# Performance work log

Hardware: AMD Instinct MI355X
Metric: run time of the kernel (lower is better)

Reference implementation:

```python
import jax, jax.numpy as jnp
import numpy as np

# fixed 9 neighborhood offsets (center + 8 directions), in pixel units
BASE = np.array([[0,0],[-1,-1],[0,-1],[1,-1],[-1,0],[1,0],[-1,1],[0,1],[1,1]], dtype=np.float32)
MAX_DELTA = 0.5 / 512.0


def bilinear_sample(vm, gx, gy):
    """vm: (D,H,W); gx,gy: (N,) normalized grid coords in [-1,1].
    Bilinear, padding_mode='zeros', align_corners=True. Returns (D,N)."""
    D, H, W = vm.shape
    ix = (gx + 1.0) * 0.5 * (W - 1)
    iy = (gy + 1.0) * 0.5 * (H - 1)
    x0 = jnp.floor(ix); y0 = jnp.floor(iy)
    x1 = x0 + 1.0;      y1 = y0 + 1.0
    wx1 = ix - x0; wx0 = 1.0 - wx1
    wy1 = iy - y0; wy0 = 1.0 - wy1
    fm = vm.reshape(D, H * W)

    def corner(xf, yf, wx, wy):
        valid = (xf >= 0) & (xf <= W - 1) & (yf >= 0) & (yf <= H - 1)
        xi = jnp.clip(xf.astype(jnp.int32), 0, W - 1)
        yi = jnp.clip(yf.astype(jnp.int32), 0, H - 1)
        v = jnp.take(fm, yi * W + xi, axis=1)  # (D,N) gather
        w = jnp.where(valid, wx * wy, 0.0)
        return v * w

    return (corner(x0, y0, wx0, wy0) + corner(x1, y0, wx1, wy0)
            + corner(x0, y1, wx0, wy1) + corner(x1, y1, wx1, wy1))


def setup_inputs() -> dict:
    key = jax.random.key(0)
    ks = jax.random.split(key, 5)
    B, C, Hf, Wf = 4, 256, 128, 128
    T, D = 16384, 128
    fmap = jax.random.normal(ks[0], (B, C, Hf, Wf), dtype=jnp.float32)
    coords = jax.random.uniform(ks[1], (B, T, 2), dtype=jnp.float32)
    W_proj = jax.random.normal(ks[2], (D, C), dtype=jnp.float32) * (1.0 / np.sqrt(C))
    W1 = jax.random.normal(ks[3], (D, D), dtype=jnp.float32) * (1.0 / np.sqrt(D))
    b1 = jnp.zeros((D,), dtype=jnp.float32)
    W2 = jax.random.normal(ks[4], (2, D), dtype=jnp.float32) * (1.0 / np.sqrt(D))
    b2 = jnp.zeros((2,), dtype=jnp.float32)
    return {"fmap": fmap, "coords": coords, "W_proj": W_proj,
            "W1": W1, "b1": b1, "W2": W2, "b2": b2}


def reference(fmap, coords, W_proj, W1, b1, W2, b2):
    B, C, Hf, Wf = fmap.shape
    T = coords.shape[1]
    K = BASE.shape[0]
    # 1x1 conv projection
    vm = jnp.einsum('bchw,dc->bdhw', fmap, W_proj)  # (B,D,Hf,Wf)
    # offsets: one pixel step in [0,1] coords (align_corners=True)
    step = jnp.array([1.0 / (Wf - 1), 1.0 / (Hf - 1)], dtype=coords.dtype)
    grid = coords[:, :, None, :] + jnp.asarray(BASE)[None, None] * step  # (B,T,K,2)
    grid = grid * 2.0 - 1.0                                            # normalize to [-1,1]
    grid = grid.reshape(B, T * K, 2)
    feat = jax.vmap(bilinear_sample)(vm, grid[..., 0], grid[..., 1])   # (B,D,T*K)
    D = feat.shape[1]
    feat = feat.transpose(0, 2, 1).reshape(B, T, K, D).mean(axis=2)    # (B,T,D)
    h = jax.nn.relu(feat @ W1.T + b1)
    delta = jnp.tanh(h @ W2.T + b2) * MAX_DELTA
    return coords + delta
```

## Files before the change

kernel.cpp:

```cpp
#include <hip/hip_runtime.h>
#include <cstddef>

#define NB 4
#define NC 256
#define ND 128
#define NH 128
#define NW 128
#define NHW (NH*NW)
#define NT 16384
#define NBKT 1024
#define CAP 192
#define FS 136

typedef short   short8  __attribute__((ext_vector_type(8)));
typedef unsigned short ushort8 __attribute__((ext_vector_type(8)));
typedef float   floatx4 __attribute__((ext_vector_type(4)));
typedef float   floatx2 __attribute__((ext_vector_type(2)));

__device__ __forceinline__ unsigned pk_bf16(float a, float b) {
    unsigned ua = __float_as_uint(a);
    unsigned ub = __float_as_uint(b);
    ua += 0x7fffu + ((ua >> 16) & 1u);
    ub += 0x7fffu + ((ub >> 16) & 1u);
    return (ua >> 16) | (ub & 0xffff0000u);
}

__device__ __forceinline__ unsigned fp8x4_from_f32(float v0, float v1, float v2, float v3) {
    int r = 0;
    r = __builtin_amdgcn_cvt_pk_fp8_f32(v0, v1, r, false);
    r = __builtin_amdgcn_cvt_pk_fp8_f32(v2, v3, r, true);
    return (unsigned)r;
}
template <bool HI>
__device__ __forceinline__ floatx2 fp8x2_to_f32(unsigned w) {
    return __builtin_amdgcn_cvt_pk_f32_fp8((int)w, HI);
}

__device__ __forceinline__ int bucket_of(float cx, float cy, int b) {
    int x0 = (int)floorf(cx * (float)(NW - 1));
    int y0 = (int)floorf(cy * (float)(NH - 1));
    x0 = min(max(x0, 0), NW - 1);
    y0 = min(max(y0, 0), NH - 1);
    return b * 256 + (y0 >> 3) * 16 + (x0 >> 3);
}

__global__ __launch_bounds__(1024)
void fill_kernel(const float* __restrict__ coords, const float* __restrict__ W1,
                 int* __restrict__ counts, int* __restrict__ order,
                 unsigned short* __restrict__ W1bf)
{
    const int bi = blockIdx.x;
    if (bi >= 64) {
        const int i = (bi - 64) * 1024 + threadIdx.x;
        unsigned u = __float_as_uint(W1[i]);
        u += 0x7fffu + ((u >> 16) & 1u);
        W1bf[i] = (unsigned short)(u >> 16);
        return;
    }
    const int g = bi * 1024 + threadIdx.x;
    const float cx = coords[(size_t)g*2 + 0];
    const float cy = coords[(size_t)g*2 + 1];
    const int bkt = bucket_of(cx, cy, g >> 14);
    const int pos = atomicAdd(&counts[bkt], 1);
    if (pos < CAP) order[bkt*CAP + pos] = g;
}

__global__ __launch_bounds__(512, 4)
void proj_kernel(const float* __restrict__ fmap, const float* __restrict__ Wp,
                 unsigned char* __restrict__ vm)
{
    const int bi = blockIdx.x;
    __shared__ unsigned short awp[8*8*64*8];

    const int t    = threadIdx.x;
    const int lane = t & 63;
    const int w    = t >> 6;
    const int l15  = lane & 15;
    const int q    = lane >> 4;
    const int cq   = q * 8;

    {
        const int dt = w;
        const float* wr0 = Wp + (size_t)(dt*16 + l15)*NC + cq;
        #pragma unroll
        for (int ch = 0; ch < 8; ++ch) {
            float4 g0 = *(const float4*)(wr0 + ch*32);
            float4 g1 = *(const float4*)(wr0 + ch*32 + 4);
            uint4 pk = make_uint4(pk_bf16(g0.x,g0.y), pk_bf16(g0.z,g0.w),
                                  pk_bf16(g1.x,g1.y), pk_bf16(g1.z,g1.w));
            *(uint4*)&awp[((dt*8 + ch)*64 + lane)*8] = pk;
        }
    }
    __syncthreads();

    const int b    = (bi & 7) >> 1;
    const int slot = ((bi >> 3) << 1) | (bi & 1);
    const int p    = slot*128 + w*16 + l15;

    floatx4 acc[8];
    #pragma unroll
    for (int i = 0; i < 8; ++i) acc[i] = (floatx4)(0.f);

    const float* fbase = fmap + (size_t)b*NC*NHW + p;

    #pragma unroll
    for (int c0 = 0; c0 < 8; ++c0) {
        const float* bp = fbase + (size_t)(c0*32 + cq)*NHW;
        float f[8];
        #pragma unroll
        for (int j = 0; j < 8; ++j) f[j] = bp[(size_t)j*NHW];
        union { short8 v; unsigned u[4]; } bc;
        #pragma unroll
        for (int j = 0; j < 4; ++j) bc.u[j] = pk_bf16(f[2*j], f[2*j+1]);
        #pragma unroll
        for (int dt = 0; dt < 8; ++dt) {
            short8 afr = *(const short8*)&awp[((dt*8 + c0)*64 + lane)*8];
            acc[dt] = __builtin_amdgcn_mfma_f32_16x16x32_bf16(afr, bc.v, acc[dt], 0, 0, 0);
        }
    }
    unsigned char* vrow = vm + ((size_t)(b*NHW + p))*ND;
    #pragma unroll
    for (int dt = 0; dt < 8; ++dt) {
        floatx4 v = acc[dt];
        *(unsigned*)&vrow[dt*16 + q*4] = fp8x4_from_f32(v[0], v[1], v[2], v[3]);
    }
}

__global__ __launch_bounds__(512, 4)
void gather_mlp(const unsigned char* __restrict__ vm, const float* __restrict__ coords,
                const int* __restrict__ counts, const int* __restrict__ order,
                const unsigned short* __restrict__ W1bf, const float* __restrict__ b1,
                const float* __restrict__ W2, const float* __restrict__ b2,
                float* __restrict__ out)
{
    __shared__ unsigned short feat[64 * FS];
    __shared__ float part[64][8];
    __shared__ float W2s[256];
    __shared__ float b1s[128];
    __shared__ int gidx[64];
    const int t   = threadIdx.x;
    const int bkt = blockIdx.x;
    const int n      = min(counts[bkt], CAP);
    const int chunks = (n + 63) >> 6;

    if (t < 128) {
        W2s[t*2]   = W2[t];
        W2s[t*2+1] = W2[ND + t];
        b1s[t]     = b1[t];
    }
    __syncthreads();

    for (int c = 0; c < chunks; ++c) {
        const int np = min(n - c*64, 64);

        {
            const int pt = t >> 3;
            const int c8 = t & 7;
            if (pt < np) {
                const int g = order[bkt*CAP + c*64 + pt];
                if (c8 == 0) gidx[pt] = g;
                const int b = g >> 14;
                const float cx = coords[(size_t)g*2 + 0];
                const float cy = coords[(size_t)g*2 + 1];
                const float ix = cx * (float)(NW - 1);
                const float iy = cy * (float)(NH - 1);
                const float x0f = floorf(ix), y0f = floorf(iy);
                const int x0 = (int)x0f, y0 = (int)y0f;
                const float wx1 = ix - x0f, wy1 = iy - y0f;
                const float wxv[4] = {1.f - wx1, 1.f, 1.f, wx1};
                const float wyv[4] = {1.f - wy1, 1.f, 1.f, wy1};
                floatx2 acc[8];
                #pragma unroll
                for (int k = 0; k < 8; ++k) acc[k] = (floatx2)(0.f);
                const unsigned char* vmb = vm + (size_t)b*NHW*ND + c8*16;
                #pragma unroll
                for (int j = 0; j < 4; ++j) {
                    const int Y  = y0 - 1 + j;
                    const int Yc = min(max(Y, 0), NH-1);
                    const bool vy = (Y >= 0) & (Y < NH);
                    #pragma unroll
                    for (int i = 0; i < 4; ++i) {
                        const int X  = x0 - 1 + i;
                        const int Xc = min(max(X, 0), NW-1);
                        const bool vx = (X >= 0) & (X < NW);
                        const float wgt = (vx & vy) ? wxv[i]*wyv[j] : 0.f;
                        uint4 u = *(const uint4*)(vmb + (size_t)(Yc*NW + Xc)*ND);
                        const floatx2 w2 = {wgt, wgt};
                        acc[0] += w2 * fp8x2_to_f32<false>(u.x);
                        acc[1] += w2 * fp8x2_to_f32<true >(u.x);
                        acc[2] += w2 * fp8x2_to_f32<false>(u.y);
                        acc[3] += w2 * fp8x2_to_f32<true >(u.y);
                        acc[4] += w2 * fp8x2_to_f32<false>(u.z);
                        acc[5] += w2 * fp8x2_to_f32<true >(u.z);
                        acc[6] += w2 * fp8x2_to_f32<false>(u.w);
                        acc[7] += w2 * fp8x2_to_f32<true >(u.w);
                    }
                }
                const float s9 = 1.f/9.f;
                unsigned pk[8];
                #pragma unroll
                for (int k = 0; k < 8; ++k)
                    pk[k] = pk_bf16(acc[k].x*s9, acc[k].y*s9);
                *(uint4*)&feat[pt*FS + c8*16]     = make_uint4(pk[0],pk[1],pk[2],pk[3]);
                *(uint4*)&feat[pt*FS + c8*16 + 8] = make_uint4(pk[4],pk[5],pk[6],pk[7]);
            }
        }
        __syncthreads();

        {
            const int lane = t & 63;
            const int w    = t >> 6;
            const int l15  = lane & 15;
            const int q    = lane >> 4;
            const int mp   = w & 3;
            const int npr  = w >> 2;

            floatx4 C[2][2];
            #pragma unroll
            for (int mi = 0; mi < 2; ++mi)
                #pragma unroll
                for (int ni = 0; ni < 2; ++ni) C[mi][ni] = (floatx4)(0.f);

            #pragma unroll
            for (int kk = 0; kk < 4; ++kk) {
                short8 a0 = *(const short8*)&W1bf[((mp*2+0)*16 + l15)*ND + kk*32 + q*8];
                short8 a1 = *(const short8*)&W1bf[((mp*2+1)*16 + l15)*ND + kk*32 + q*8];
                short8 f0 = *(const short8*)&feat[((npr*2+0)*16 + l15)*FS + kk*32 + q*8];
                short8 f1 = *(const short8*)&feat[((npr*2+1)*16 + l15)*FS + kk*32 + q*8];
                C[0][0] = __builtin_amdgcn_mfma_f32_16x16x32_bf16(a0, f0, C[0][0], 0, 0, 0);
                C[0][1] = __builtin_amdgcn_mfma_f32_16x16x32_bf16(a0, f1, C[0][1], 0, 0, 0);
                C[1][0] = __builtin_amdgcn_mfma_f32_16x16x32_bf16(a1, f0, C[1][0], 0, 0, 0);
                C[1][1] = __builtin_amdgcn_mfma_f32_16x16x32_bf16(a1, f1, C[1][1], 0, 0, 0);
            }
            #pragma unroll
            for (int ni = 0; ni < 2; ++ni) {
                float s0 = 0.f, s1 = 0.f;
                #pragma unroll
                for (int mi = 0; mi < 2; ++mi) {
                    const int e0 = (mp*2 + mi)*16 + q*4;
                    float4 bq = *(const float4*)&b1s[e0];
                    floatx4 h4 = C[mi][ni];
                    #pragma unroll
                    for (int r = 0; r < 4; ++r) {
                        float hv = fmaxf(h4[r] + (&bq.x)[r], 0.f);
                        float2 wv = *(const float2*)&W2s[(e0 + r)*2];
                        s0 = fmaf(hv, wv.x, s0);
                        s1 = fmaf(hv, wv.y, s1);
                    }
                }
                s0 += __shfl_xor(s0, 16); s0 += __shfl_xor(s0, 32);
                s1 += __shfl_xor(s1, 16); s1 += __shfl_xor(s1, 32);
                if (q == 0) {
                    const int pt = (npr*2 + ni)*16 + l15;
                    part[pt][mp*2 + 0] = s0;
                    part[pt][mp*2 + 1] = s1;
                }
            }
        }
        __syncthreads();

        if (t < np) {
            const int g = gidx[t];
            float s0 = part[t][0] + part[t][2] + part[t][4] + part[t][6];
            float s1 = part[t][1] + part[t][3] + part[t][5] + part[t][7];
            const float cx = coords[(size_t)g*2 + 0];
            const float cy = coords[(size_t)g*2 + 1];
            const float MD = 0.5f / 512.0f;
            float2 o = make_float2(cx + tanhf(s0 + b2[0]) * MD,
                                   cy + tanhf(s1 + b2[1]) * MD);
            *(float2*)&out[(size_t)g*2] = o;
        }
        __syncthreads();
    }
}

extern "C" void kernel_launch(void* const* d_in, const int* in_sizes, int n_in,
                              void* d_out, int out_size, void* d_ws, size_t ws_size,
                              hipStream_t stream)
{
    const float* fmap   = (const float*)d_in[0];
    const float* coords = (const float*)d_in[1];
    const float* Wp     = (const float*)d_in[2];
    const float* W1     = (const float*)d_in[3];
    const float* b1     = (const float*)d_in[4];
    const float* W2     = (const float*)d_in[5];
    const float* b2     = (const float*)d_in[6];
    float* out = (float*)d_out;

    unsigned char* vm = (unsigned char*)d_ws;
    char* base = (char*)d_ws + (size_t)NB*NHW*ND;
    unsigned short* W1bf = (unsigned short*)base;
    int* counts = (int*)(base + 32768);
    int* order  = (int*)(base + 32768 + 4096);

    hipMemsetAsync(counts, 0, NBKT*sizeof(int), stream);
    fill_kernel<<<dim3(64 + 16), 1024, 0, stream>>>(coords, W1, counts, order, W1bf);
    proj_kernel<<<dim3(512),      512, 0, stream>>>(fmap, Wp, vm);
    gather_mlp <<<dim3(NBKT),     512, 0, stream>>>(vm, coords, counts, order,
                                                    W1bf, b1, W2, b2, out);
}
```

Measured before the change: 152.6 us.

## Split bucket chunks into a work queue and precompute bf16 projection weights

Each bucket's chunks of up to 64 points now become separate queue entries, built by an extra block in the projection kernel. The gather/MLP kernel launches one block per queue entry instead of looping over chunks inside one block per bucket, which spreads uneven bucket loads across more blocks. The fp32-to-bf16 conversion and swizzle of the projection weights moves into the fill kernel, so each projection block only copies the packed weights into shared memory. In exchange it adds a queue-building pass and atomics, launches up to 3072 blocks that early-exit when unused, and spends extra workspace.

```diff
diff --git a/kernel.cpp b/kernel.cpp
--- a/kernel.cpp
+++ b/kernel.cpp
@@ -11,6 +11,7 @@
 #define NBKT 1024
 #define CAP 192
 #define FS 136
+#define MAXQ 3072
 
 typedef short   short8  __attribute__((ext_vector_type(8)));
 typedef unsigned short ushort8 __attribute__((ext_vector_type(8)));
@@ -46,18 +47,34 @@
 
 __global__ __launch_bounds__(1024)
 void fill_kernel(const float* __restrict__ coords, const float* __restrict__ W1,
+                 const float* __restrict__ Wp,
                  int* __restrict__ counts, int* __restrict__ order,
-                 unsigned short* __restrict__ W1bf)
+                 unsigned short* __restrict__ W1bf, unsigned short* __restrict__ Wpbf)
 {
     const int bi = blockIdx.x;
+    const int t  = threadIdx.x;
+    if (bi >= 80) {
+        const int idx  = (bi - 80) * 1024 + t;
+        const int lane = idx & 63;
+        const int ch   = (idx >> 6) & 7;
+        const int dt   = idx >> 9;
+        const int l15  = lane & 15;
+        const int q    = lane >> 4;
+        const float* src = Wp + (size_t)(dt*16 + l15)*NC + ch*32 + q*8;
+        float4 g0 = *(const float4*)src;
+        float4 g1 = *(const float4*)(src + 4);
+        *(uint4*)&Wpbf[idx*8] = make_uint4(pk_bf16(g0.x,g0.y), pk_bf16(g0.z,g0.w),
+                                           pk_bf16(g1.x,g1.y), pk_bf16(g1.z,g1.w));
+        return;
+    }
     if (bi >= 64) {
-        const int i = (bi - 64) * 1024 + threadIdx.x;
+        const int i = (bi - 64) * 1024 + t;
         unsigned u = __float_as_uint(W1[i]);
         u += 0x7fffu + ((u >> 16) & 1u);
         W1bf[i] = (unsigned short)(u >> 16);
         return;
     }
-    const int g = bi * 1024 + threadIdx.x;
+    const int g = bi * 1024 + t;
     const float cx = coords[(size_t)g*2 + 0];
     const float cy = coords[(size_t)g*2 + 1];
     const int bkt = bucket_of(cx, cy, g >> 14);
@@ -66,32 +83,43 @@
 }
 
 __global__ __launch_bounds__(512, 4)
-void proj_kernel(const float* __restrict__ fmap, const float* __restrict__ Wp,
-                 unsigned char* __restrict__ vm)
+void proj_kernel(const float* __restrict__ fmap, const unsigned short* __restrict__ Wpbf,
+                 const int* __restrict__ counts, int* __restrict__ queue,
+                 int* __restrict__ qlen, unsigned char* __restrict__ vm)
 {
     const int bi = blockIdx.x;
+    const int t  = threadIdx.x;
+
+    if (bi == 512) {
+        for (int bkt = t; bkt < NBKT; bkt += 512) {
+            const int n  = min(counts[bkt], CAP);
+            const int nc = (n + 63) >> 6;
+            if (nc > 0) {
+                const int pos = atomicAdd(qlen, nc);
+                for (int cc = 0; cc < nc; ++cc) {
+                    const int np = min(n - cc*64, 64);
+                    queue[pos + cc] = bkt | (cc << 10) | (np << 16);
+                }
+            }
+        }
+        return;
+    }
+
     __shared__ unsigned short awp[8*8*64*8];
 
-    const int t    = threadIdx.x;
+    {
+        const uint4* src = (const uint4*)Wpbf;
+        uint4* dst = (uint4*)awp;
+        #pragma unroll
+        for (int i = 0; i < 8; ++i) dst[t + i*512] = src[t + i*512];
+    }
+    __syncthreads();
+
     const int lane = t & 63;
     const int w    = t >> 6;
     const int l15  = lane & 15;
     const int q    = lane >> 4;
     const int cq   = q * 8;
-
-    {
-        const int dt = w;
-        const float* wr0 = Wp + (size_t)(dt*16 + l15)*NC + cq;
-        #pragma unroll
-        for (int ch = 0; ch < 8; ++ch) {
-            float4 g0 = *(const float4*)(wr0 + ch*32);
-            float4 g1 = *(const float4*)(wr0 + ch*32 + 4);
-            uint4 pk = make_uint4(pk_bf16(g0.x,g0.y), pk_bf16(g0.z,g0.w),
-                                  pk_bf16(g1.x,g1.y), pk_bf16(g1.z,g1.w));
-            *(uint4*)&awp[((dt*8 + ch)*64 + lane)*8] = pk;
-        }
-    }
-    __syncthreads();
 
     const int b    = (bi & 7) >> 1;
     const int slot = ((bi >> 3) << 1) | (bi & 1);
@@ -128,7 +156,8 @@
 
 __global__ __launch_bounds__(512, 4)
 void gather_mlp(const unsigned char* __restrict__ vm, const float* __restrict__ coords,
-                const int* __restrict__ counts, const int* __restrict__ order,
+                const int* __restrict__ order, const int* __restrict__ queue,
+                const int* __restrict__ qlen,
                 const unsigned short* __restrict__ W1bf, const float* __restrict__ b1,
                 const float* __restrict__ W2, const float* __restrict__ b2,
                 float* __restrict__ out)
@@ -138,83 +167,83 @@
     __shared__ float W2s[256];
     __shared__ float b1s[128];
     __shared__ int gidx[64];
+
+    if (blockIdx.x >= qlen[0]) return;
+    const int e   = queue[blockIdx.x];
+    const int bkt = e & 1023;
+    const int c   = (e >> 10) & 3;
+    const int np  = e >> 16;
     const int t   = threadIdx.x;
-    const int bkt = blockIdx.x;
-    const int n      = min(counts[bkt], CAP);
-    const int chunks = (n + 63) >> 6;
 
     if (t < 128) {
         W2s[t*2]   = W2[t];
         W2s[t*2+1] = W2[ND + t];
         b1s[t]     = b1[t];
     }
+
+    {
+        const int pt = t >> 3;
+        const int c8 = t & 7;
+        if (pt < np) {
+            const int g = order[bkt*CAP + c*64 + pt];
+            if (c8 == 0) gidx[pt] = g;
+            const int b = g >> 14;
+            const float cx = coords[(size_t)g*2 + 0];
+            const float cy = coords[(size_t)g*2 + 1];
+            const float ix = cx * (float)(NW - 1);
+            const float iy = cy * (float)(NH - 1);
+            const float x0f = floorf(ix), y0f = floorf(iy);
+            const int x0 = (int)x0f, y0 = (int)y0f;
+            const float wx1 = ix - x0f, wy1 = iy - y0f;
+            const float wxv[4] = {1.f - wx1, 1.f, 1.f, wx1};
+            const float wyv[4] = {1.f - wy1, 1.f, 1.f, wy1};
+            floatx2 acc[8];
+            #pragma unroll
+            for (int k = 0; k < 8; ++k) acc[k] = (floatx2)(0.f);
+            const unsigned char* vmb = vm + (size_t)b*NHW*ND + c8*16;
+            #pragma unroll
+            for (int j = 0; j < 4; ++j) {
+                const int Y  = y0 - 1 + j;
+                const int Yc = min(max(Y, 0), NH-1);
+                const bool vy = (Y >= 0) & (Y < NH);
+                #pragma unroll
+                for (int i = 0; i < 4; ++i) {
+                    const int X  = x0 - 1 + i;
+                    const int Xc = min(max(X, 0), NW-1);
+                    const bool vx = (X >= 0) & (X < NW);
+                    const float wgt = (vx & vy) ? wxv[i]*wyv[j] : 0.f;
+                    uint4 u = *(const uint4*)(vmb + (size_t)(Yc*NW + Xc)*ND);
+                    const floatx2 w2 = {wgt, wgt};
+                    acc[0] += w2 * fp8x2_to_f32<false>(u.x);
+                    acc[1] += w2 * fp8x2_to_f32<true >(u.x);
+                    acc[2] += w2 * fp8x2_to_f32<false>(u.y);
+                    acc[3] += w2 * fp8x2_to_f32<true >(u.y);
+                    acc[4] += w2 * fp8x2_to_f32<false>(u.z);
+                    acc[5] += w2 * fp8x2_to_f32<true >(u.z);
+                    acc[6] += w2 * fp8x2_to_f32<false>(u.w);
+                    acc[7] += w2 * fp8x2_to_f32<true >(u.w);
+                }
+            }
+            const float s9 = 1.f/9.f;
+            unsigned pk[8];
+            #pragma unroll
+            for (int k = 0; k < 8; ++k)
+                pk[k] = pk_bf16(acc[k].x*s9, acc[k].y*s9);
+            *(uint4*)&feat[pt*FS + c8*16]     = make_uint4(pk[0],pk[1],pk[2],pk[3]);
+            *(uint4*)&feat[pt*FS + c8*16 + 8] = make_uint4(pk[4],pk[5],pk[6],pk[7]);
+        }
+    }
     __syncthreads();
 
-    for (int c = 0; c < chunks; ++c) {
-        const int np = min(n - c*64, 64);
-
-        {
-            const int pt = t >> 3;
-            const int c8 = t & 7;
-            if (pt < np) {
-                const int g = order[bkt*CAP + c*64 + pt];
-                if (c8 == 0) gidx[pt] = g;
-                const int b = g >> 14;
-                const float cx = coords[(size_t)g*2 + 0];
-                const float cy = coords[(size_t)g*2 + 1];
-                const float ix = cx * (float)(NW - 1);
-                const float iy = cy * (float)(NH - 1);
-                const float x0f = floorf(ix), y0f = floorf(iy);
-                const int x0 = (int)x0f, y0 = (int)y0f;
-                const float wx1 = ix - x0f, wy1 = iy - y0f;
-                const float wxv[4] = {1.f - wx1, 1.f, 1.f, wx1};
-                const float wyv[4] = {1.f - wy1, 1.f, 1.f, wy1};
-                floatx2 acc[8];
-                #pragma unroll
-                for (int k = 0; k < 8; ++k) acc[k] = (floatx2)(0.f);
-                const unsigned char* vmb = vm + (size_t)b*NHW*ND + c8*16;
-                #pragma unroll
-                for (int j = 0; j < 4; ++j) {
-                    const int Y  = y0 - 1 + j;
-                    const int Yc = min(max(Y, 0), NH-1);
-                    const bool vy = (Y >= 0) & (Y < NH);
-                    #pragma unroll
-                    for (int i = 0; i < 4; ++i) {
-                        const int X  = x0 - 1 + i;
-                        const int Xc = min(max(X, 0), NW-1);
-                        const bool vx = (X >= 0) & (X < NW);
-                        const float wgt = (vx & vy) ? wxv[i]*wyv[j] : 0.f;
-                        uint4 u = *(const uint4*)(vmb + (size_t)(Yc*NW + Xc)*ND);
-                        const floatx2 w2 = {wgt, wgt};
-                        acc[0] += w2 * fp8x2_to_f32<false>(u.x);
-                        acc[1] += w2 * fp8x2_to_f32<true >(u.x);
-                        acc[2] += w2 * fp8x2_to_f32<false>(u.y);
-                        acc[3] += w2 * fp8x2_to_f32<true >(u.y);
-                        acc[4] += w2 * fp8x2_to_f32<false>(u.z);
-                        acc[5] += w2 * fp8x2_to_f32<true >(u.z);
-                        acc[6] += w2 * fp8x2_to_f32<false>(u.w);
-                        acc[7] += w2 * fp8x2_to_f32<true >(u.w);
-                    }
-                }
-                const float s9 = 1.f/9.f;
-                unsigned pk[8];
-                #pragma unroll
-                for (int k = 0; k < 8; ++k)
-                    pk[k] = pk_bf16(acc[k].x*s9, acc[k].y*s9);
-                *(uint4*)&feat[pt*FS + c8*16]     = make_uint4(pk[0],pk[1],pk[2],pk[3]);
-                *(uint4*)&feat[pt*FS + c8*16 + 8] = make_uint4(pk[4],pk[5],pk[6],pk[7]);
-            }
-        }
-        __syncthreads();
-
-        {
-            const int lane = t & 63;
-            const int w    = t >> 6;
-            const int l15  = lane & 15;
-            const int q    = lane >> 4;
-            const int mp   = w & 3;
-            const int npr  = w >> 2;
-
+    {
+        const int lane = t & 63;
+        const int w    = t >> 6;
+        const int l15  = lane & 15;
+        const int q    = lane >> 4;
+        const int mp   = w & 3;
+        const int npr  = w >> 2;
+
+        if (npr*32 < np) {
             floatx4 C[2][2];
             #pragma unroll
             for (int mi = 0; mi < 2; ++mi)
@@ -257,20 +286,19 @@
                 }
             }
         }
-        __syncthreads();
-
-        if (t < np) {
-            const int g = gidx[t];
-            float s0 = part[t][0] + part[t][2] + part[t][4] + part[t][6];
-            float s1 = part[t][1] + part[t][3] + part[t][5] + part[t][7];
-            const float cx = coords[(size_t)g*2 + 0];
-            const float cy = coords[(size_t)g*2 + 1];
-            const float MD = 0.5f / 512.0f;
-            float2 o = make_float2(cx + tanhf(s0 + b2[0]) * MD,
-                                   cy + tanhf(s1 + b2[1]) * MD);
-            *(float2*)&out[(size_t)g*2] = o;
-        }
-        __syncthreads();
+    }
+    __syncthreads();
+
+    if (t < np) {
+        const int g = gidx[t];
+        float s0 = part[t][0] + part[t][2] + part[t][4] + part[t][6];
+        float s1 = part[t][1] + part[t][3] + part[t][5] + part[t][7];
+        const float cx = coords[(size_t)g*2 + 0];
+        const float cy = coords[(size_t)g*2 + 1];
+        const float MD = 0.5f / 512.0f;
+        float2 o = make_float2(cx + tanhf(s0 + b2[0]) * MD,
+                               cy + tanhf(s1 + b2[1]) * MD);
+        *(float2*)&out[(size_t)g*2] = o;
     }
 }
 
@@ -290,12 +318,16 @@
     unsigned char* vm = (unsigned char*)d_ws;
     char* base = (char*)d_ws + (size_t)NB*NHW*ND;
     unsigned short* W1bf = (unsigned short*)base;
-    int* counts = (int*)(base + 32768);
-    int* order  = (int*)(base + 32768 + 4096);
-
-    hipMemsetAsync(counts, 0, NBKT*sizeof(int), stream);
-    fill_kernel<<<dim3(64 + 16), 1024, 0, stream>>>(coords, W1, counts, order, W1bf);
-    proj_kernel<<<dim3(512),      512, 0, stream>>>(fmap, Wp, vm);
-    gather_mlp <<<dim3(NBKT),     512, 0, stream>>>(vm, coords, counts, order,
-                                                    W1bf, b1, W2, b2, out);
-}
+    unsigned short* Wpbf = (unsigned short*)(base + 32768);
+    int* counts = (int*)(base + 98304);
+    int* qlen   = (int*)(base + 102400);
+    int* queue  = (int*)(base + 102416);
+    int* order  = (int*)(base + 114704);
+
+    hipMemsetAsync(counts, 0, NBKT*sizeof(int) + 16, stream);
+    fill_kernel<<<dim3(64 + 16 + 4), 1024, 0, stream>>>(coords, W1, Wp, counts, order,
+                                                        W1bf, Wpbf);
+    proj_kernel<<<dim3(513),  512, 0, stream>>>(fmap, Wpbf, counts, queue, qlen, vm);
+    gather_mlp <<<dim3(MAXQ), 512, 0, stream>>>(vm, coords, order, queue, qlen,
+                                                W1bf, b1, W2, b2, out);
+}
```

Result: faster. 145.6 us (-4.6%).

## Fuse bucketing into projection kernel and split gather chunks across blocks

Applied to the files above, without the earlier changes.

Folds the coordinate bucketing and the W1 bf16 conversion into the projection kernel, using spare threads in each block, which removes one kernel launch. The gather/MLP kernel now gives each 64-point chunk of a bucket its own block (a 3072-block grid with early exit for empty chunks) instead of looping over chunks serially inside one block. It also skips MFMA work for warps whose point rows are all empty. The risks are many idle blocks that launch and exit at once, and extra per-block setup for the W2/b1 loads.

```diff
diff --git a/kernel.cpp b/kernel.cpp
--- a/kernel.cpp
+++ b/kernel.cpp
@@ -11,6 +11,7 @@
 #define NBKT 1024
 #define CAP 192
 #define FS 136
+#define GGRID 3072
 
 typedef short   short8  __attribute__((ext_vector_type(8)));
 typedef unsigned short ushort8 __attribute__((ext_vector_type(8)));
@@ -44,35 +45,31 @@
     return b * 256 + (y0 >> 3) * 16 + (x0 >> 3);
 }
 
-__global__ __launch_bounds__(1024)
-void fill_kernel(const float* __restrict__ coords, const float* __restrict__ W1,
-                 int* __restrict__ counts, int* __restrict__ order,
-                 unsigned short* __restrict__ W1bf)
+__global__ __launch_bounds__(512, 4)
+void proj_fused(const float* __restrict__ fmap, const float* __restrict__ coords,
+                const float* __restrict__ Wp, const float* __restrict__ W1,
+                int* __restrict__ counts, int* __restrict__ order,
+                unsigned short* __restrict__ W1bf, unsigned char* __restrict__ vm)
 {
     const int bi = blockIdx.x;
-    if (bi >= 64) {
-        const int i = (bi - 64) * 1024 + threadIdx.x;
+    const int t  = threadIdx.x;
+
+    if (t < 128) {
+        const int g = bi * 128 + t;
+        const float cx = coords[(size_t)g*2 + 0];
+        const float cy = coords[(size_t)g*2 + 1];
+        const int bkt = bucket_of(cx, cy, g >> 14);
+        const int pos = atomicAdd(&counts[bkt], 1);
+        if (pos < CAP) order[bkt*CAP + pos] = g;
+    } else if (t < 160) {
+        const int i = bi * 32 + (t - 128);
         unsigned u = __float_as_uint(W1[i]);
         u += 0x7fffu + ((u >> 16) & 1u);
         W1bf[i] = (unsigned short)(u >> 16);
-        return;
-    }
-    const int g = bi * 1024 + threadIdx.x;
-    const float cx = coords[(size_t)g*2 + 0];
-    const float cy = coords[(size_t)g*2 + 1];
-    const int bkt = bucket_of(cx, cy, g >> 14);
-    const int pos = atomicAdd(&counts[bkt], 1);
-    if (pos < CAP) order[bkt*CAP + pos] = g;
-}
-
-__global__ __launch_bounds__(512, 4)
-void proj_kernel(const float* __restrict__ fmap, const float* __restrict__ Wp,
-                 unsigned char* __restrict__ vm)
-{
-    const int bi = blockIdx.x;
+    }
+
     __shared__ unsigned short awp[8*8*64*8];
 
-    const int t    = threadIdx.x;
     const int lane = t & 63;
     const int w    = t >> 6;
     const int l15  = lane & 15;
@@ -138,83 +135,83 @@
     __shared__ float W2s[256];
     __shared__ float b1s[128];
     __shared__ int gidx[64];
+
+    const int bkt = blockIdx.x & 1023;
+    const int c   = blockIdx.x >> 10;
+    const int n   = min(counts[bkt], CAP);
+    const int np  = min(n - c*64, 64);
+    if (np <= 0) return;
     const int t   = threadIdx.x;
-    const int bkt = blockIdx.x;
-    const int n      = min(counts[bkt], CAP);
-    const int chunks = (n + 63) >> 6;
 
     if (t < 128) {
         W2s[t*2]   = W2[t];
         W2s[t*2+1] = W2[ND + t];
         b1s[t]     = b1[t];
     }
+
+    {
+        const int pt = t >> 3;
+        const int c8 = t & 7;
+        if (pt < np) {
+            const int g = order[bkt*CAP + c*64 + pt];
+            if (c8 == 0) gidx[pt] = g;
+            const int b = g >> 14;
+            const float cx = coords[(size_t)g*2 + 0];
+            const float cy = coords[(size_t)g*2 + 1];
+            const float ix = cx * (float)(NW - 1);
+            const float iy = cy * (float)(NH - 1);
+            const float x0f = floorf(ix), y0f = floorf(iy);
+            const int x0 = (int)x0f, y0 = (int)y0f;
+            const float wx1 = ix - x0f, wy1 = iy - y0f;
+            const float wxv[4] = {1.f - wx1, 1.f, 1.f, wx1};
+            const float wyv[4] = {1.f - wy1, 1.f, 1.f, wy1};
+            floatx2 acc[8];
+            #pragma unroll
+            for (int k = 0; k < 8; ++k) acc[k] = (floatx2)(0.f);
+            const unsigned char* vmb = vm + (size_t)b*NHW*ND + c8*16;
+            #pragma unroll
+            for (int j = 0; j < 4; ++j) {
+                const int Y  = y0 - 1 + j;
+                const int Yc = min(max(Y, 0), NH-1);
+                const bool vy = (Y >= 0) & (Y < NH);
+                #pragma unroll
+                for (int i = 0; i < 4; ++i) {
+                    const int X  = x0 - 1 + i;
+                    const int Xc = min(max(X, 0), NW-1);
+                    const bool vx = (X >= 0) & (X < NW);
+                    const float wgt = (vx & vy) ? wxv[i]*wyv[j] : 0.f;
+                    uint4 u = *(const uint4*)(vmb + (size_t)(Yc*NW + Xc)*ND);
+                    const floatx2 w2 = {wgt, wgt};
+                    acc[0] += w2 * fp8x2_to_f32<false>(u.x);
+                    acc[1] += w2 * fp8x2_to_f32<true >(u.x);
+                    acc[2] += w2 * fp8x2_to_f32<false>(u.y);
+                    acc[3] += w2 * fp8x2_to_f32<true >(u.y);
+                    acc[4] += w2 * fp8x2_to_f32<false>(u.z);
+                    acc[5] += w2 * fp8x2_to_f32<true >(u.z);
+                    acc[6] += w2 * fp8x2_to_f32<false>(u.w);
+                    acc[7] += w2 * fp8x2_to_f32<true >(u.w);
+                }
+            }
+            const float s9 = 1.f/9.f;
+            unsigned pk[8];
+            #pragma unroll
+            for (int k = 0; k < 8; ++k)
+                pk[k] = pk_bf16(acc[k].x*s9, acc[k].y*s9);
+            *(uint4*)&feat[pt*FS + c8*16]     = make_uint4(pk[0],pk[1],pk[2],pk[3]);
+            *(uint4*)&feat[pt*FS + c8*16 + 8] = make_uint4(pk[4],pk[5],pk[6],pk[7]);
+        }
+    }
     __syncthreads();
 
-    for (int c = 0; c < chunks; ++c) {
-        const int np = min(n - c*64, 64);
-
-        {
-            const int pt = t >> 3;
-            const int c8 = t & 7;
-            if (pt < np) {
-                const int g = order[bkt*CAP + c*64 + pt];
-                if (c8 == 0) gidx[pt] = g;
-                const int b = g >> 14;
-                const float cx = coords[(size_t)g*2 + 0];
-                const float cy = coords[(size_t)g*2 + 1];
-                const float ix = cx * (float)(NW - 1);
-                const float iy = cy * (float)(NH - 1);
-                const float x0f = floorf(ix), y0f = floorf(iy);
-                const int x0 = (int)x0f, y0 = (int)y0f;
-                const float wx1 = ix - x0f, wy1 = iy - y0f;
-                const float wxv[4] = {1.f - wx1, 1.f, 1.f, wx1};
-                const float wyv[4] = {1.f - wy1, 1.f, 1.f, wy1};
-                floatx2 acc[8];
-                #pragma unroll
-                for (int k = 0; k < 8; ++k) acc[k] = (floatx2)(0.f);
-                const unsigned char* vmb = vm + (size_t)b*NHW*ND + c8*16;
-                #pragma unroll
-                for (int j = 0; j < 4; ++j) {
-                    const int Y  = y0 - 1 + j;
-                    const int Yc = min(max(Y, 0), NH-1);
-                    const bool vy = (Y >= 0) & (Y < NH);
-                    #pragma unroll
-                    for (int i = 0; i < 4; ++i) {
-                        const int X  = x0 - 1 + i;
-                        const int Xc = min(max(X, 0), NW-1);
-                        const bool vx = (X >= 0) & (X < NW);
-                        const float wgt = (vx & vy) ? wxv[i]*wyv[j] : 0.f;
-                        uint4 u = *(const uint4*)(vmb + (size_t)(Yc*NW + Xc)*ND);
-                        const floatx2 w2 = {wgt, wgt};
-                        acc[0] += w2 * fp8x2_to_f32<false>(u.x);
-                        acc[1] += w2 * fp8x2_to_f32<true >(u.x);
-                        acc[2] += w2 * fp8x2_to_f32<false>(u.y);
-                        acc[3] += w2 * fp8x2_to_f32<true >(u.y);
-                        acc[4] += w2 * fp8x2_to_f32<false>(u.z);
-                        acc[5] += w2 * fp8x2_to_f32<true >(u.z);
-                        acc[6] += w2 * fp8x2_to_f32<false>(u.w);
-                        acc[7] += w2 * fp8x2_to_f32<true >(u.w);
-                    }
-                }
-                const float s9 = 1.f/9.f;
-                unsigned pk[8];
-                #pragma unroll
-                for (int k = 0; k < 8; ++k)
-                    pk[k] = pk_bf16(acc[k].x*s9, acc[k].y*s9);
-                *(uint4*)&feat[pt*FS + c8*16]     = make_uint4(pk[0],pk[1],pk[2],pk[3]);
-                *(uint4*)&feat[pt*FS + c8*16 + 8] = make_uint4(pk[4],pk[5],pk[6],pk[7]);
-            }
-        }
-        __syncthreads();
-
-        {
-            const int lane = t & 63;
-            const int w    = t >> 6;
-            const int l15  = lane & 15;
-            const int q    = lane >> 4;
-            const int mp   = w & 3;
-            const int npr  = w >> 2;
-
+    {
+        const int lane = t & 63;
+        const int w    = t >> 6;
+        const int l15  = lane & 15;
+        const int q    = lane >> 4;
+        const int mp   = w & 3;
+        const int npr  = w >> 2;
+
+        if (npr*32 < np) {
             floatx4 C[2][2];
             #pragma unroll
             for (int mi = 0; mi < 2; ++mi)
@@ -257,20 +254,19 @@
                 }
             }
         }
-        __syncthreads();
-
-        if (t < np) {
-            const int g = gidx[t];
-            float s0 = part[t][0] + part[t][2] + part[t][4] + part[t][6];
-            float s1 = part[t][1] + part[t][3] + part[t][5] + part[t][7];
-            const float cx = coords[(size_t)g*2 + 0];
-            const float cy = coords[(size_t)g*2 + 1];
-            const float MD = 0.5f / 512.0f;
-            float2 o = make_float2(cx + tanhf(s0 + b2[0]) * MD,
-                                   cy + tanhf(s1 + b2[1]) * MD);
-            *(float2*)&out[(size_t)g*2] = o;
-        }
-        __syncthreads();
+    }
+    __syncthreads();
+
+    if (t < np) {
+        const int g = gidx[t];
+        float s0 = part[t][0] + part[t][2] + part[t][4] + part[t][6];
+        float s1 = part[t][1] + part[t][3] + part[t][5] + part[t][7];
+        const float cx = coords[(size_t)g*2 + 0];
+        const float cy = coords[(size_t)g*2 + 1];
+        const float MD = 0.5f / 512.0f;
+        float2 o = make_float2(cx + tanhf(s0 + b2[0]) * MD,
+                               cy + tanhf(s1 + b2[1]) * MD);
+        *(float2*)&out[(size_t)g*2] = o;
     }
 }
 
@@ -294,8 +290,8 @@
     int* order  = (int*)(base + 32768 + 4096);
 
     hipMemsetAsync(counts, 0, NBKT*sizeof(int), stream);
-    fill_kernel<<<dim3(64 + 16), 1024, 0, stream>>>(coords, W1, counts, order, W1bf);
-    proj_kernel<<<dim3(512),      512, 0, stream>>>(fmap, Wp, vm);
-    gather_mlp <<<dim3(NBKT),     512, 0, stream>>>(vm, coords, counts, order,
-                                                    W1bf, b1, W2, b2, out);
-}
+    proj_fused<<<dim3(512),   512, 0, stream>>>(fmap, coords, Wp, W1,
+                                                counts, order, W1bf, vm);
+    gather_mlp<<<dim3(GGRID), 512, 0, stream>>>(vm, coords, counts, order,
+                                                W1bf, b1, W2, b2, out);
+}
```

New measurement: 145.0 us. -5.0%, faster.
